# Kernel optimization log

Hardware: AMD Instinct MI355X
Metric: run time of the kernel (lower is better)

The kernel has to match this reference:

```python
import jax, jax.numpy as jnp
import numpy as np

T, B, H = 512, 256, 512

def setup_inputs() -> dict:
    key = jax.random.key(0)
    k1, k2, k3, k4 = jax.random.split(key, 4)
    inputs = jax.random.normal(k1, (T, B, H), jnp.float32)
    resets = jax.random.randint(k2, (T, B), 0, 2).astype(bool)
    # flax OptimizedLSTMCell params: fused 4H gate projections (gate order i, f, g, o)
    scale = 1.0 / np.sqrt(H).astype(np.float32)
    Wi = jax.random.normal(k3, (H, 4 * H), jnp.float32) * scale  # input kernel (no bias)
    Wh = jax.random.normal(k4, (H, 4 * H), jnp.float32) * scale  # hidden kernel
    b = jnp.zeros((4 * H,), jnp.float32)                         # hidden bias
    c0 = jnp.zeros((B, H), jnp.float32)
    h0 = jnp.zeros((B, H), jnp.float32)
    return {"inputs": inputs, "resets": resets, "c0": c0, "h0": h0,
            "Wi": Wi, "Wh": Wh, "b": b}

def reference(inputs, resets, c0, h0, Wi, Wh, b):
    # inputs: [T, B, H], resets: [T, B] bool. initialize_carry is zeros, so
    # the reset masking zeroes (c, h) where resets is True before the cell step.
    def step(carry, xt):
        c, h = carry
        x, r = xt
        m = r[:, None]
        c = jnp.where(m, 0.0, c)
        h = jnp.where(m, 0.0, h)
        gates = x @ Wi + h @ Wh + b           # [B, 4H]
        i, f, g, o = jnp.split(gates, 4, axis=-1)
        c_new = jax.nn.sigmoid(f) * c + jax.nn.sigmoid(i) * jnp.tanh(g)
        h_new = jax.nn.sigmoid(o) * jnp.tanh(c_new)
        return (c_new, h_new), h_new
    (c_f, h_f), ys = jax.lax.scan(step, (c0, h0), (inputs, resets))
    return ys, c_f, h_f
```

## Files before the change

kernel.cpp:

```cpp
#include <hip/hip_runtime.h>

#define TT 512
#define BB 256
#define HH 512
#define FH 2048

typedef __attribute__((ext_vector_type(8))) short short8;
typedef __attribute__((ext_vector_type(4))) short short4v;
typedef __attribute__((ext_vector_type(4))) float f32x4;
typedef __attribute__((ext_vector_type(2))) float f32x2;

__device__ __forceinline__ short f2bf(float f) {
  union { float f; unsigned u; } v; v.f = f;
  unsigned r = v.u + 0x7fffu + ((v.u >> 16) & 1u);
  return (short)(r >> 16);
}
__device__ __forceinline__ unsigned short f2h(float f) {
  union { _Float16 h; unsigned short u; } v;
  v.h = (_Float16)f;
  return v.u;
}
__device__ __forceinline__ float h2f(unsigned short u) {
  union { _Float16 h; unsigned short u; } v;
  v.u = u;
  return (float)v.h;
}

__device__ __forceinline__ float sigm(float x) {
  return 1.f / (1.f + __expf(-x));
}
__device__ __forceinline__ float tanh_fast(float x) {
  float e = __expf(2.f * x);
  return 1.f - 2.f / (e + 1.f);
}

__device__ __forceinline__ void gload16(const void* g, void* l) {
  __builtin_amdgcn_global_load_lds(
      (const __attribute__((address_space(1))) unsigned*)g,
      (__attribute__((address_space(3))) unsigned*)(unsigned)(unsigned long long)l,
      16, 0, 0);
}

__global__ __launch_bounds__(256) void prep_w(
    const float* __restrict__ Wi, const float* __restrict__ Wh,
    short* __restrict__ WiT, short* __restrict__ WhT) {
  __shared__ short t[64][65];
  const int w = blockIdx.x >> 8;
  const int tile = blockIdx.x & 255;
  const int c0 = (tile & 31) * 64;
  const int k0 = (tile >> 5) * 64;
  const float* src = w ? Wh : Wi;
  short* dst = w ? WhT : WiT;
  const int tid = threadIdx.x;

  {
    const int r = tid >> 2;
    const int cq = (tid & 3) * 16;
#pragma unroll
    for (int i = 0; i < 4; ++i) {
      f32x4 v = *(const f32x4*)(src + (size_t)(k0 + r) * FH + c0 + cq + i * 4);
      short4v s = { f2bf(v[0]), f2bf(v[1]), f2bf(v[2]), f2bf(v[3]) };
      *(short4v*)(&t[r][cq + i * 4]) = s;
    }
  }
  __syncthreads();

  {
    const int c = tid >> 2;
    const int kq = (tid & 3) * 16;
    short8 o0, o1;
#pragma unroll
    for (int e = 0; e < 8; ++e) {
      o0[e] = t[kq + e][c];
      o1[e] = t[kq + 8 + e][c];
    }
    short* d = dst + (size_t)(c0 + c) * 512 + k0 + kq;
    *(short8*)d = o0;
    *(short8*)(d + 8) = o1;
  }
}

__global__ void prep_kernel(const float* __restrict__ h0, const float* __restrict__ c0,
                            const float* __restrict__ x,
                            unsigned* __restrict__ hb0, float* __restrict__ cb,
                            short* __restrict__ hbf, short* __restrict__ Xb,
                            int* __restrict__ done) {
  int idx = blockIdx.x * blockDim.x + threadIdx.x;
  int stride = gridDim.x * blockDim.x;
  for (int i = idx; i < BB * HH; i += stride) {
    hbf[i] = f2bf(h0[i]);
    cb[i] = c0[i];
  }
  for (int i = idx; i < BB * 256; i += stride) {
    int row = i >> 8;
    int cpx = (i & 255) * 2;
    hb0[i] = (unsigned)(unsigned short)f2bf(h0[(size_t)row * HH + cpx]) |
             ((unsigned)(unsigned short)f2bf(h0[(size_t)row * HH + cpx + 1]) << 16);
  }
  for (int i = idx; i < 8 * TT * 32; i += stride) done[i] = 0;
  const size_t nx4 = (size_t)TT * BB * HH / 4;
  for (size_t i = idx; i < nx4; i += stride) {
    f32x4 v = *(const f32x4*)(x + i * 4);
    short4v s = { f2bf(v[0]), f2bf(v[1]), f2bf(v[2]), f2bf(v[3]) };
    *(short4v*)(Xb + i * 4) = s;
  }
}

__global__ __launch_bounds__(256) void precomp_kernel(
    const short* __restrict__ Xb, const short* __restrict__ WiT,
    const float* __restrict__ bias, unsigned short* __restrict__ Gx,
    int rowBase) {
  __shared__ short As[128 * 64];
  __shared__ short Bs[128 * 64];

  const int tid = threadIdx.x;

  int coltile, rowtile;
  if ((gridDim.x & 127) == 0) {
    const int b = blockIdx.x;
    const int xcd = b & 7;
    const int i = b >> 3;
    rowtile = (i >> 4) * 8 + xcd;
    coltile = i & 15;
  } else {
    coltile = blockIdx.x & 15;
    rowtile = blockIdx.x >> 4;
  }
  const int cb0 = coltile * 128;
  const int rb = rowtile * 128;
  const size_t grow = (size_t)rowBase + rb;

  const int wid = tid >> 6;
  const int lane = tid & 63;
  const int lc = lane & 15;
  const int kg = lane >> 4;
  const int m0 = (wid >> 1) * 64;
  const int n0 = (wid & 1) * 64;

  const int srow0 = wid * 32;
  const int lrow = lane >> 3;
  const int lkc = lane & 7;

  f32x4 acc[4][4] = {};

  for (int kt = 0; kt < 8; ++kt) {
    const int k0 = kt * 64;
    __syncthreads();
#pragma unroll
    for (int i = 0; i < 4; ++i) {
      const int row = srow0 + i * 8 + lrow;
      gload16(Xb + (grow + row) * 512 + k0 + lkc * 8,
              (char*)As + (size_t)(srow0 + i * 8) * 128);
      gload16(WiT + (size_t)(cb0 + row) * 512 + k0 + lkc * 8,
              (char*)Bs + (size_t)(srow0 + i * 8) * 128);
    }
    __syncthreads();

#pragma unroll
    for (int ks = 0; ks < 2; ++ks) {
      const int kb = ks * 64 + kg * 16;
      short8 af[4], bf[4];
#pragma unroll
      for (int m = 0; m < 4; ++m)
        af[m] = *(const short8*)((char*)As + (m0 + m * 16 + lc) * 128 + kb);
#pragma unroll
      for (int n = 0; n < 4; ++n)
        bf[n] = *(const short8*)((char*)Bs + (n0 + n * 16 + lc) * 128 + kb);
#pragma unroll
      for (int m = 0; m < 4; ++m)
#pragma unroll
        for (int n = 0; n < 4; ++n)
          acc[m][n] = __builtin_amdgcn_mfma_f32_16x16x32_bf16(af[m], bf[n],
                                                              acc[m][n], 0, 0, 0);
    }
  }

#pragma unroll
  for (int n = 0; n < 4; ++n) {
    const int col = cb0 + n0 + n * 16 + lc;
    const float bv = bias[col];
#pragma unroll
    for (int m = 0; m < 4; ++m) {
      const int rloc = rb + m0 + m * 16 + kg * 4;
#pragma unroll
      for (int j = 0; j < 4; ++j)
        Gx[(size_t)(rloc + j) * FH + col] = f2h(acc[m][n][j] + bv);
    }
  }
}

__global__ __launch_bounds__(256) void lstm_persist(
    const int* __restrict__ resets,
    const short* __restrict__ WhT,
    const unsigned short* __restrict__ Gx,
    unsigned* __restrict__ hbA,
    unsigned* __restrict__ hbB,
    float* __restrict__ cb,
    float* __restrict__ out,
    int* __restrict__ done,
    int t0, int ct) {
  extern __shared__ short whs[];
  __shared__ short ah[32 * 512];
  __shared__ float gex[4 * 32 * 17];

  const int tid = threadIdx.x;
  const int bid = blockIdx.x;
  const int grp = bid >> 5;
  const int j = bid & 31;
  const int rb = grp * 32;
  const int hc0 = j * 16;

  const int wid = tid >> 6;
  const int lane = tid & 63;
  const int lc = lane & 15;
  const int kg = lane >> 4;

  {
    const int lcol = tid >> 2;
    const int part = tid & 3;
    const int g = lcol >> 4;
    const int gcol = g * 512 + hc0 + (lcol & 15);
    const short* src = WhT + (size_t)gcol * 512 + part * 128;
    const int dbase = lcol * 1024 + part * 256;
    const int sw = (lcol & 7) << 4;
#pragma unroll
    for (int it = 0; it < 16; ++it) {
      short8 v = *(const short8*)(src + it * 8);
      *(short8*)((char*)whs + ((dbase + it * 16) ^ sw)) = v;
    }
  }

  const int erow = tid >> 3;
  const int cp = (tid & 7) * 2;
  float creg[2];
  {
    const float* cs = cb + (size_t)(rb + erow) * HH + hc0 + cp;
    creg[0] = cs[0];
    creg[1] = cs[1];
  }

  __syncthreads();

  for (int t = t0; t < t0 + ct; ++t) {
    const unsigned short* gxb =
        Gx + ((size_t)(t - t0) * BB + (rb + erow)) * FH + hc0 + cp;
    unsigned gxu[4];
#pragma unroll
    for (int g = 0; g < 4; ++g) gxu[g] = *(const unsigned*)(gxb + g * 512);
    const int* rstT = resets + (size_t)t * BB;
    const int rstE = rstT[rb + erow];

    if (t > t0) {
      if (wid == 0) {
        int* dn = done + ((size_t)grp * TT + (t - 1)) * 32;
        bool ok;
        do {
          int v = (lane < 32)
                      ? __hip_atomic_load(&dn[lane], __ATOMIC_RELAXED,
                                          __HIP_MEMORY_SCOPE_AGENT)
                      : 1;
          ok = __all(v != 0);
          if (!ok) __builtin_amdgcn_s_sleep(2);
        } while (!ok);
      }
      __syncthreads();
    }

    {
      unsigned* hsrc = ((t & 1) ? hbB : hbA) + (size_t)rb * 256;
      unsigned hv[32];
#pragma unroll
      for (int it = 0; it < 32; ++it)
        hv[it] = __hip_atomic_load(&hsrc[it * 256 + tid], __ATOMIC_RELAXED,
                                   __HIP_MEMORY_SCOPE_AGENT);
#pragma unroll
      for (int it = 0; it < 32; ++it) {
        unsigned v = (rstT[rb + it] != 0) ? 0u : hv[it];
        *(unsigned*)((char*)ah + ((it * 1024 + tid * 4) ^ ((it & 7) << 4))) = v;
      }
    }
    __syncthreads();

    {
      const int sw = (lc & 7) << 4;
      f32x4 acc[2] = {};
#pragma unroll
      for (int kk = 0; kk < 16; ++kk) {
        const int kb = kk * 64 + kg * 16;
        short8 a0 = *(const short8*)((char*)ah + ((lc * 1024 + kb) ^ sw));
        short8 a1 = *(const short8*)((char*)ah + (((lc + 16) * 1024 + kb) ^ sw));
        short8 b = *(const short8*)((char*)whs +
                      (((wid * 16 + lc) * 1024 + kb) ^ sw));
        acc[0] = __builtin_amdgcn_mfma_f32_16x16x32_bf16(a0, b, acc[0], 0, 0, 0);
        acc[1] = __builtin_amdgcn_mfma_f32_16x16x32_bf16(a1, b, acc[1], 0, 0, 0);
      }
#pragma unroll
      for (int m = 0; m < 2; ++m)
#pragma unroll
        for (int jj = 0; jj < 4; ++jj)
          gex[wid * 544 + (m * 16 + kg * 4 + jj) * 17 + lc] = acc[m][jj];
    }
    __syncthreads();

    {
      unsigned* hdst = (t & 1) ? hbA : hbB;
      const int gb = erow * 17 + cp;
      float gi0 = gex[0 * 544 + gb] + h2f((unsigned short)(gxu[0] & 0xffffu));
      float gi1 = gex[0 * 544 + gb + 1] + h2f((unsigned short)(gxu[0] >> 16));
      float gf0 = gex[1 * 544 + gb] + h2f((unsigned short)(gxu[1] & 0xffffu));
      float gf1 = gex[1 * 544 + gb + 1] + h2f((unsigned short)(gxu[1] >> 16));
      float gg0 = gex[2 * 544 + gb] + h2f((unsigned short)(gxu[2] & 0xffffu));
      float gg1 = gex[2 * 544 + gb + 1] + h2f((unsigned short)(gxu[2] >> 16));
      float go0 = gex[3 * 544 + gb] + h2f((unsigned short)(gxu[3] & 0xffffu));
      float go1 = gex[3 * 544 + gb + 1] + h2f((unsigned short)(gxu[3] >> 16));
      float cold0 = rstE ? 0.f : creg[0];
      float cold1 = rstE ? 0.f : creg[1];
      float cn0 = sigm(gf0) * cold0 + sigm(gi0) * tanh_fast(gg0);
      float cn1 = sigm(gf1) * cold1 + sigm(gi1) * tanh_fast(gg1);
      float hn0 = sigm(go0) * tanh_fast(cn0);
      float hn1 = sigm(go1) * tanh_fast(cn1);
      creg[0] = cn0;
      creg[1] = cn1;
      unsigned pack = (unsigned)(unsigned short)f2bf(hn0) |
                      ((unsigned)(unsigned short)f2bf(hn1) << 16);
      __hip_atomic_store(&hdst[(size_t)(rb + erow) * 256 + (hc0 >> 1) + (tid & 7)],
                         pack, __ATOMIC_RELAXED, __HIP_MEMORY_SCOPE_AGENT);
      asm volatile("s_waitcnt vmcnt(0)" ::: "memory");
      __syncthreads();
      if (tid == 0)
        __hip_atomic_store(&done[((size_t)grp * TT + t) * 32 + j], 1,
                           __ATOMIC_RELAXED, __HIP_MEMORY_SCOPE_AGENT);
      size_t gidx = (size_t)(rb + erow) * HH + hc0 + cp;
      *(f32x2*)(out + (size_t)t * BB * HH + gidx) = (f32x2){hn0, hn1};
      if (t == TT - 1) {
        out[(size_t)TT * BB * HH + gidx] = cn0;
        out[(size_t)TT * BB * HH + gidx + 1] = cn1;
        out[(size_t)TT * BB * HH + (size_t)BB * HH + gidx] = hn0;
        out[(size_t)TT * BB * HH + (size_t)BB * HH + gidx + 1] = hn1;
      }
    }
  }

  {
    float* cs = cb + (size_t)(rb + erow) * HH + hc0 + cp;
    cs[0] = creg[0];
    cs[1] = creg[1];
  }
}

__global__ __launch_bounds__(64) void lstm_step_fullk(
    const float* __restrict__ xt, const int* __restrict__ rst,
    const float* __restrict__ bias, const short* __restrict__ WiT,
    const short* __restrict__ WhT, const short* __restrict__ hin,
    short* __restrict__ hout, float* __restrict__ cbuf, float* __restrict__ ys) {
  const int lane = threadIdx.x;
  const int lc = lane & 15;
  const int kg = lane >> 4;
  const int r0 = blockIdx.x * 16;
  const int h0 = blockIdx.y * 16;
  const int hc = h0 + lc;

  float coldv[4];
  int rstj[4];
#pragma unroll
  for (int jj = 0; jj < 4; ++jj) {
    int row = r0 + kg * 4 + jj;
    rstj[jj] = rst[row];
    coldv[jj] = cbuf[(size_t)row * HH + hc];
  }

  const int rowA = r0 + lc;
  const bool rm = rst[rowA] != 0;
  const short8 zero = {};
  f32x4 acc[4] = {};
#pragma unroll
  for (int kk = 0; kk < 16; ++kk) {
    const int ko = kk * 32 + kg * 8;
    f32x4 u0 = *(const f32x4*)(xt + (size_t)rowA * HH + ko);
    f32x4 u1 = *(const f32x4*)(xt + (size_t)rowA * HH + ko + 4);
    short8 a;
#pragma unroll
    for (int e = 0; e < 4; ++e) { a[e] = f2bf(u0[e]); a[e + 4] = f2bf(u1[e]); }
#pragma unroll
    for (int g = 0; g < 4; ++g) {
      const short8 b = *(const short8*)(WiT + (size_t)(g * HH + h0 + lc) * HH + ko);
      acc[g] = __builtin_amdgcn_mfma_f32_16x16x32_bf16(a, b, acc[g], 0, 0, 0);
    }
  }
#pragma unroll
  for (int kk = 0; kk < 16; ++kk) {
    const int ko = kk * 32 + kg * 8;
    short8 a = rm ? zero : *(const short8*)(hin + (size_t)rowA * HH + ko);
#pragma unroll
    for (int g = 0; g < 4; ++g) {
      const short8 b = *(const short8*)(WhT + (size_t)(g * HH + h0 + lc) * HH + ko);
      acc[g] = __builtin_amdgcn_mfma_f32_16x16x32_bf16(a, b, acc[g], 0, 0, 0);
    }
  }

#pragma unroll
  for (int jj = 0; jj < 4; ++jj) {
    int row = r0 + kg * 4 + jj;
    float gi = acc[0][jj] + bias[0 * HH + hc];
    float gf = acc[1][jj] + bias[1 * HH + hc];
    float gg = acc[2][jj] + bias[2 * HH + hc];
    float go = acc[3][jj] + bias[3 * HH + hc];
    float cold = rstj[jj] ? 0.f : coldv[jj];
    float cn = sigm(gf) * cold + sigm(gi) * tanh_fast(gg);
    float hn = sigm(go) * tanh_fast(cn);
    cbuf[(size_t)row * HH + hc] = cn;
    hout[(size_t)row * HH + hc] = f2bf(hn);
    ys[(size_t)row * HH + hc] = hn;
  }
}

__global__ void finalize_kernel(const float* __restrict__ cbuf, float* __restrict__ out) {
  int i = blockIdx.x * blockDim.x + threadIdx.x;
  if (i < BB * HH) {
    size_t base = (size_t)TT * BB * HH;
    out[base + i] = cbuf[i];
    out[base + BB * HH + i] = out[(size_t)(TT - 1) * BB * HH + i];
  }
}

extern "C" void kernel_launch(void* const* d_in, const int* in_sizes, int n_in,
                              void* d_out, int out_size, void* d_ws, size_t ws_size,
                              hipStream_t stream) {
  const float* x      = (const float*)d_in[0];
  const int*   resets = (const int*)d_in[1];
  const float* c0     = (const float*)d_in[2];
  const float* h0     = (const float*)d_in[3];
  const float* Wi     = (const float*)d_in[4];
  const float* Wh     = (const float*)d_in[5];
  const float* bias   = (const float*)d_in[6];
  float* out = (float*)d_out;

  char* ws = (char*)d_ws;
  short* WiT = (short*)ws;
  short* WhT = (short*)(ws + (2u << 20));
  unsigned* hb0 = (unsigned*)(ws + (4u << 20));
  unsigned* hb1 = (unsigned*)(ws + (4u << 20) + (256u << 10));
  float* cb  = (float*)(ws + (4u << 20) + (512u << 10));
  short* hbf0 = (short*)(ws + (5u << 20));
  short* hbf1 = hbf0 + BB * HH;
  int*   dn  = (int*)(ws + (5u << 20) + (512u << 10));
  short* Xb  = (short*)(ws + (6u << 20));
  const size_t GX_OFF = (6u << 20) + (size_t)TT * BB * HH * 2;
  unsigned short* Gx = (unsigned short*)(ws + GX_OFF);

  const size_t perT = (size_t)BB * FH * 2;
  int chunkT = 0;
  if (ws_size > GX_OFF + perT) chunkT = (int)((ws_size - GX_OFF) / perT);
  if (chunkT > TT) chunkT = TT;
  chunkT &= ~3;

  prep_w<<<512, 256, 0, stream>>>(Wi, Wh, WiT, WhT);
  prep_kernel<<<2048, 256, 0, stream>>>(h0, c0, x, hb0, cb, hbf0, Xb, dn);

  if (chunkT >= 4) {
    for (int t0 = 0; t0 < TT; t0 += chunkT) {
      int ct = (TT - t0 < chunkT) ? (TT - t0) : chunkT;
      precomp_kernel<<<ct * 32, 256, 0, stream>>>(Xb, WiT, bias, Gx, t0 * BB);
      lstm_persist<<<256, 256, 65536, stream>>>(resets, WhT, Gx, hb0, hb1,
                                                cb, out, dn, t0, ct);
    }
  } else {
    for (int t = 0; t < TT; ++t) {
      const short* hin = (t & 1) ? hbf1 : hbf0;
      short* hout      = (t & 1) ? hbf0 : hbf1;
      lstm_step_fullk<<<dim3(16, 32), 64, 0, stream>>>(
          x + (size_t)t * BB * HH, resets + (size_t)t * BB, bias, WiT, WhT,
          hin, hout, cb, out + (size_t)t * BB * HH);
    }
    finalize_kernel<<<(BB * HH + 255) / 256, 256, 0, stream>>>(cb, out);
  }
}
```

Measured before the change: 2.390 ms.

## Fuse input bf16 conversion into precompute GEMM and use counter barrier

```diff
diff --git a/kernel.cpp b/kernel.cpp
--- a/kernel.cpp
+++ b/kernel.cpp
@@ -32,13 +32,6 @@
 __device__ __forceinline__ float tanh_fast(float x) {
   float e = __expf(2.f * x);
   return 1.f - 2.f / (e + 1.f);
-}
-
-__device__ __forceinline__ void gload16(const void* g, void* l) {
-  __builtin_amdgcn_global_load_lds(
-      (const __attribute__((address_space(1))) unsigned*)g,
-      (__attribute__((address_space(3))) unsigned*)(unsigned)(unsigned long long)l,
-      16, 0, 0);
 }
 
 __global__ __launch_bounds__(256) void prep_w(
@@ -81,10 +74,8 @@
 }
 
 __global__ void prep_kernel(const float* __restrict__ h0, const float* __restrict__ c0,
-                            const float* __restrict__ x,
                             unsigned* __restrict__ hb0, float* __restrict__ cb,
-                            short* __restrict__ hbf, short* __restrict__ Xb,
-                            int* __restrict__ done) {
+                            short* __restrict__ hbf, int* __restrict__ cnt) {
   int idx = blockIdx.x * blockDim.x + threadIdx.x;
   int stride = gridDim.x * blockDim.x;
   for (int i = idx; i < BB * HH; i += stride) {
@@ -97,17 +88,11 @@
     hb0[i] = (unsigned)(unsigned short)f2bf(h0[(size_t)row * HH + cpx]) |
              ((unsigned)(unsigned short)f2bf(h0[(size_t)row * HH + cpx + 1]) << 16);
   }
-  for (int i = idx; i < 8 * TT * 32; i += stride) done[i] = 0;
-  const size_t nx4 = (size_t)TT * BB * HH / 4;
-  for (size_t i = idx; i < nx4; i += stride) {
-    f32x4 v = *(const f32x4*)(x + i * 4);
-    short4v s = { f2bf(v[0]), f2bf(v[1]), f2bf(v[2]), f2bf(v[3]) };
-    *(short4v*)(Xb + i * 4) = s;
-  }
+  for (int i = idx; i < 8 * TT; i += stride) cnt[i] = 0;
 }
 
 __global__ __launch_bounds__(256) void precomp_kernel(
-    const short* __restrict__ Xb, const short* __restrict__ WiT,
+    const float* __restrict__ X, const short* __restrict__ WiT,
     const float* __restrict__ bias, unsigned short* __restrict__ Gx,
     int rowBase) {
   __shared__ short As[128 * 64];
@@ -137,10 +122,6 @@
   const int m0 = (wid >> 1) * 64;
   const int n0 = (wid & 1) * 64;
 
-  const int srow0 = wid * 32;
-  const int lrow = lane >> 3;
-  const int lkc = lane & 7;
-
   f32x4 acc[4][4] = {};
 
   for (int kt = 0; kt < 8; ++kt) {
@@ -148,24 +129,33 @@
     __syncthreads();
 #pragma unroll
     for (int i = 0; i < 4; ++i) {
-      const int row = srow0 + i * 8 + lrow;
-      gload16(Xb + (grow + row) * 512 + k0 + lkc * 8,
-              (char*)As + (size_t)(srow0 + i * 8) * 128);
-      gload16(WiT + (size_t)(cb0 + row) * 512 + k0 + lkc * 8,
-              (char*)Bs + (size_t)(srow0 + i * 8) * 128);
+      const int idx = tid * 4 + i;
+      const int row = idx >> 3;
+      const int kc = idx & 7;
+      const float* ap = X + (grow + row) * 512 + k0 + kc * 8;
+      f32x4 u0 = *(const f32x4*)ap;
+      f32x4 u1 = *(const f32x4*)(ap + 4);
+      short8 av;
+#pragma unroll
+      for (int e = 0; e < 4; ++e) { av[e] = f2bf(u0[e]); av[e + 4] = f2bf(u1[e]); }
+      short8 bv = *(const short8*)(WiT + (size_t)(cb0 + row) * 512 + k0 + kc * 8);
+      const int off = (row * 128 + kc * 16) ^ ((row & 7) << 4);
+      *(short8*)((char*)As + off) = av;
+      *(short8*)((char*)Bs + off) = bv;
     }
     __syncthreads();
 
+    const int sw = (lc & 7) << 4;
 #pragma unroll
     for (int ks = 0; ks < 2; ++ks) {
       const int kb = ks * 64 + kg * 16;
       short8 af[4], bf[4];
 #pragma unroll
       for (int m = 0; m < 4; ++m)
-        af[m] = *(const short8*)((char*)As + (m0 + m * 16 + lc) * 128 + kb);
+        af[m] = *(const short8*)((char*)As + (((m0 + m * 16 + lc) * 128 + kb) ^ sw));
 #pragma unroll
       for (int n = 0; n < 4; ++n)
-        bf[n] = *(const short8*)((char*)Bs + (n0 + n * 16 + lc) * 128 + kb);
+        bf[n] = *(const short8*)((char*)Bs + (((n0 + n * 16 + lc) * 128 + kb) ^ sw));
 #pragma unroll
       for (int m = 0; m < 4; ++m)
 #pragma unroll
@@ -197,7 +187,7 @@
     unsigned* __restrict__ hbB,
     float* __restrict__ cb,
     float* __restrict__ out,
-    int* __restrict__ done,
+    int* __restrict__ cnt,
     int t0, int ct) {
   extern __shared__ short whs[];
   __shared__ short ah[32 * 512];
@@ -252,16 +242,10 @@
 
     if (t > t0) {
       if (wid == 0) {
-        int* dn = done + ((size_t)grp * TT + (t - 1)) * 32;
-        bool ok;
-        do {
-          int v = (lane < 32)
-                      ? __hip_atomic_load(&dn[lane], __ATOMIC_RELAXED,
-                                          __HIP_MEMORY_SCOPE_AGENT)
-                      : 1;
-          ok = __all(v != 0);
-          if (!ok) __builtin_amdgcn_s_sleep(2);
-        } while (!ok);
+        const int* cw = &cnt[grp * TT + (t - 1)];
+        while (__hip_atomic_load(cw, __ATOMIC_RELAXED,
+                                 __HIP_MEMORY_SCOPE_AGENT) < 32)
+          __builtin_amdgcn_s_sleep(1);
       }
       __syncthreads();
     }
@@ -328,8 +312,8 @@
       asm volatile("s_waitcnt vmcnt(0)" ::: "memory");
       __syncthreads();
       if (tid == 0)
-        __hip_atomic_store(&done[((size_t)grp * TT + t) * 32 + j], 1,
-                           __ATOMIC_RELAXED, __HIP_MEMORY_SCOPE_AGENT);
+        __hip_atomic_fetch_add(&cnt[grp * TT + t], 1, __ATOMIC_RELAXED,
+                               __HIP_MEMORY_SCOPE_AGENT);
       size_t gidx = (size_t)(rb + erow) * HH + hc0 + cp;
       *(f32x2*)(out + (size_t)t * BB * HH + gidx) = (f32x2){hn0, hn1};
       if (t == TT - 1) {
@@ -443,9 +427,8 @@
   float* cb  = (float*)(ws + (4u << 20) + (512u << 10));
   short* hbf0 = (short*)(ws + (5u << 20));
   short* hbf1 = hbf0 + BB * HH;
-  int*   dn  = (int*)(ws + (5u << 20) + (512u << 10));
-  short* Xb  = (short*)(ws + (6u << 20));
-  const size_t GX_OFF = (6u << 20) + (size_t)TT * BB * HH * 2;
+  int*   cnt = (int*)(ws + (5u << 20) + (512u << 10));
+  const size_t GX_OFF = (6u << 20);
   unsigned short* Gx = (unsigned short*)(ws + GX_OFF);
 
   const size_t perT = (size_t)BB * FH * 2;
@@ -455,14 +438,15 @@
   chunkT &= ~3;
 
   prep_w<<<512, 256, 0, stream>>>(Wi, Wh, WiT, WhT);
-  prep_kernel<<<2048, 256, 0, stream>>>(h0, c0, x, hb0, cb, hbf0, Xb, dn);
+  prep_kernel<<<512, 256, 0, stream>>>(h0, c0, hb0, cb, hbf0, cnt);
 
   if (chunkT >= 4) {
     for (int t0 = 0; t0 < TT; t0 += chunkT) {
       int ct = (TT - t0 < chunkT) ? (TT - t0) : chunkT;
-      precomp_kernel<<<ct * 32, 256, 0, stream>>>(Xb, WiT, bias, Gx, t0 * BB);
+      precomp_kernel<<<ct * 32, 256, 0, stream>>>(x, WiT, bias, Gx,
+                                                  t0 * BB);
       lstm_persist<<<256, 256, 65536, stream>>>(resets, WhT, Gx, hb0, hb1,
-                                                cb, out, dn, t0, ct);
+                                                cb, out, cnt, t0, ct);
     }
   } else {
     for (int t = 0; t < TT; ++t) {
```

New measurement: 2.527 ms. 5.7% more time.
